# Performance work log

Hardware: AMD Instinct MI355X
Metric: run time of the kernel (lower is better)

The kernel has to match this reference:

```python
import jax, jax.numpy as jnp
import numpy as np

N_NODES = 100000

def _sage_conv(x, src, dst, W_l, b_l, W_r):
    # PyG SAGEConv(aggr='mean'): out = lin_l(mean_{j in N(i)} x_j) + lin_r(x_i)
    agg = jax.ops.segment_sum(x[src], dst, num_segments=N_NODES)          # [N, F]
    cnt = jax.ops.segment_sum(jnp.ones_like(dst, dtype=x.dtype), dst,
                              num_segments=N_NODES)                        # [N]
    mean = agg / jnp.maximum(cnt, 1.0)[:, None]
    return mean @ W_l + b_l + x @ W_r

def setup_inputs() -> dict:
    key = jax.random.key(0)
    ks = jax.random.split(key, 10)
    F_in, H = 128, 16
    E, P = 1600000, 2000000
    x = jax.random.normal(ks[0], (N_NODES, F_in), dtype=jnp.float32)
    edge_index = jax.random.randint(ks[1], (2, E), 0, N_NODES, dtype=jnp.int64)
    decode_index = jax.random.randint(ks[2], (2, P), 0, N_NODES, dtype=jnp.int64)
    s1 = 1.0 / np.sqrt(F_in)
    s2 = 1.0 / np.sqrt(H)
    W1l = jax.random.uniform(ks[3], (F_in, H), jnp.float32, -s1, s1)
    b1 = jax.random.uniform(ks[4], (H,), jnp.float32, -s1, s1)
    W1r = jax.random.uniform(ks[5], (F_in, H), jnp.float32, -s1, s1)
    W2l = jax.random.uniform(ks[6], (H, H), jnp.float32, -s2, s2)
    b2 = jax.random.uniform(ks[7], (H,), jnp.float32, -s2, s2)
    W2r = jax.random.uniform(ks[8], (H, H), jnp.float32, -s2, s2)
    return {"x": x, "W1l": W1l, "b1": b1, "W1r": W1r,
            "W2l": W2l, "b2": b2, "W2r": W2r,
            "edge_index": edge_index, "decode_index": decode_index}

def reference(x, W1l, b1, W1r, W2l, b2, W2r, edge_index, decode_index):
    src, dst = edge_index[0], edge_index[1]
    h = _sage_conv(x, src, dst, W1l, b1, W1r)          # conv1
    h = jax.nn.relu(h)                                  # relu (dropout: eval -> identity)
    h = _sage_conv(h, src, dst, W2l, b2, W2r)           # conv2
    logits = jnp.sum(h[decode_index[0]] * h[decode_index[1]], axis=1)  # [P]
    return jax.nn.sigmoid(logits)
```

## Files before the change

### kernel.cpp

```cpp
#include <hip/hip_runtime.h>
#include <hip/hip_fp16.h>

#define N_NODES 100000
#define F_IN 128
#define H 16
#define NBIN 391
#define BINCAP 4608
#define ECHUNK 4096

__global__ void __launch_bounds__(512) k_init(int* __restrict__ binCur) {
  int t = threadIdx.x;
  if (t < NBIN) binCur[t] = t * BINCAP;
}

__global__ void __launch_bounds__(256) k_lin1(
    const float* __restrict__ x, const float* __restrict__ W1l,
    const float* __restrict__ W1r, __half* __restrict__ y1l,
    float* __restrict__ y1r) {
  __shared__ float red[2 * H * 128];
  int t = threadIdx.x;
  int part = __builtin_amdgcn_readfirstlane(t >> 7);
  int ln = t & 127;
  int n = blockIdx.x * 128 + ln;
  int nc = (n < N_NODES) ? n : (N_NODES - 1);
  const float4* xr = (const float4*)(x + (size_t)nc * F_IN + part * (F_IN / 2));
  float4 xv[16];
#pragma unroll
  for (int j = 0; j < 16; ++j) xv[j] = xr[j];
  const float* Wl = W1l + part * (F_IN / 2) * H;
  const float* Wr = W1r + part * (F_IN / 2) * H;
  float al[H], ar[H];
#pragma unroll
  for (int c = 0; c < H; ++c) { al[c] = 0.f; ar[c] = 0.f; }
#pragma unroll
  for (int j = 0; j < 16; ++j) {
    float xs[4] = {xv[j].x, xv[j].y, xv[j].z, xv[j].w};
#pragma unroll
    for (int jj = 0; jj < 4; ++jj) {
      int k = j * 4 + jj;
#pragma unroll
      for (int c = 0; c < H; ++c) {
        al[c] = fmaf(xs[jj], Wl[k * H + c], al[c]);
        ar[c] = fmaf(xs[jj], Wr[k * H + c], ar[c]);
      }
    }
  }
  if (part == 1) {
#pragma unroll
    for (int c = 0; c < H; ++c) {
      red[c * 128 + ln] = al[c];
      red[(H + c) * 128 + ln] = ar[c];
    }
  }
  __syncthreads();
  if (part == 0 && n < N_NODES) {
#pragma unroll
    for (int c = 0; c < H; ++c) {
      al[c] += red[c * 128 + ln];
      ar[c] += red[(H + c) * 128 + ln];
    }
    __half2 hp[8];
#pragma unroll
    for (int q = 0; q < 8; ++q) hp[q] = __floats2half2_rn(al[2 * q], al[2 * q + 1]);
    uint4* ol = (uint4*)(y1l + (size_t)n * H);
    ol[0] = *(uint4*)&hp[0];
    ol[1] = *(uint4*)&hp[4];
    float4* orr = (float4*)(y1r + (size_t)n * H);
#pragma unroll
    for (int q = 0; q < 4; ++q)
      orr[q] = make_float4(ar[4 * q], ar[4 * q + 1], ar[4 * q + 2], ar[4 * q + 3]);
  }
}

__global__ void __launch_bounds__(512) k_binfill(
    const int* __restrict__ src, const int* __restrict__ dst,
    int* __restrict__ binCur, int* __restrict__ recs, int E) {
  __shared__ int hist[512];
  __shared__ int gbase[512];
  __shared__ int cnt2[512];
  int t = threadIdx.x;
  hist[t] = 0;
  cnt2[t] = 0;
  __syncthreads();
  int base = blockIdx.x * ECHUNK;
  int rec[8], bin[8];
#pragma unroll
  for (int j = 0; j < 8; ++j) {
    int e = base + j * 512 + t;
    if (e < E) {
      int s = src[e];
      int d = dst[e];
      rec[j] = (s << 8) | (d & 255);
      bin[j] = d >> 8;
      atomicAdd(&hist[bin[j]], 1);
    } else {
      bin[j] = -1;
    }
  }
  __syncthreads();
  if (t < NBIN) {
    int c = hist[t];
    gbase[t] = (c > 0) ? atomicAdd(&binCur[t], c) : 0;
  }
  __syncthreads();
#pragma unroll
  for (int j = 0; j < 8; ++j) {
    if (bin[j] >= 0) {
      int loc = atomicAdd(&cnt2[bin[j]], 1);
      int slot = gbase[bin[j]] + loc;
      if (slot < (bin[j] + 1) * BINCAP)
        recs[slot] = rec[j];
    }
  }
}

__global__ void __launch_bounds__(512) k_binsort(
    int* __restrict__ recs, const int* __restrict__ binCur,
    int* __restrict__ deg, int* __restrict__ rowBeg) {
  __shared__ int lrec[BINCAP];
  __shared__ int srtg[BINCAP];
  __shared__ int hist[256];
  __shared__ int off[256];
  __shared__ int cur[256];
  int t = threadIdx.x;
  int b = blockIdx.x;
  int rbase = b * BINCAP;
  int R = binCur[b] - rbase;
  if (R > BINCAP) R = BINCAP;
  if (t < 256) hist[t] = 0;
  __syncthreads();
#pragma unroll
  for (int j = 0; j < 9; ++j) {
    int idx = j * 512 + t;
    if (idx < R) {
      int r = recs[rbase + idx];
      lrec[idx] = r;
      atomicAdd(&hist[r & 255], 1);
    }
  }
  __syncthreads();
  if (t < 256) off[t] = hist[t];
  __syncthreads();
  for (int o = 1; o < 256; o <<= 1) {
    int u = 0;
    if (t < 256 && t >= o) u = off[t - o];
    __syncthreads();
    if (t < 256) off[t] += u;
    __syncthreads();
  }
  if (t < 256) {
    int ex = off[t] - hist[t];
    cur[t] = ex;
    int n = (b << 8) + t;
    if (n < N_NODES) {
      deg[n] = hist[t];
      rowBeg[n] = rbase + ex;
    }
  }
  __syncthreads();
#pragma unroll
  for (int j = 0; j < 9; ++j) {
    int idx = j * 512 + t;
    if (idx < R) {
      int r = lrec[idx];
      int slot = atomicAdd(&cur[r & 255], 1);
      srtg[slot] = r;
    }
  }
  __syncthreads();
#pragma unroll
  for (int j = 0; j < 9; ++j) {
    int idx = j * 512 + t;
    if (idx < R) {
      int r = srtg[idx];
      int node = r & 255;
      int ex = off[node] - hist[node];
      int cnt = hist[node];
      int rank = 0;
      for (int k = ex; k < ex + cnt; ++k) {
        int v = srtg[k];
        rank += (v < r) || (v == r && k < idx);
      }
      lrec[ex + rank] = r >> 8;
    }
  }
  __syncthreads();
#pragma unroll
  for (int j = 0; j < 9; ++j) {
    int idx = j * 512 + t;
    if (idx < R) recs[rbase + idx] = lrec[idx];
  }
}

__global__ void __launch_bounds__(256) k_gather1(
    const int* __restrict__ srcSorted, const int* __restrict__ deg,
    const int* __restrict__ rowBeg, const __half* __restrict__ y1l,
    const float* __restrict__ y1r, const float* __restrict__ b1,
    const float* __restrict__ W2l, const float* __restrict__ W2r,
    __half* __restrict__ z2l, float* __restrict__ z2r) {
  int tid = blockIdx.x * 256 + threadIdx.x;
  int n = tid >> 2;
  int q = tid & 3;
  if (n >= N_NODES) return;
  int beg = rowBeg[n];
  int dg = deg[n];
  int end = beg + dg;
  float acc0 = 0.f, acc1 = 0.f, acc2 = 0.f, acc3 = 0.f;
  int i = beg;
  for (; i + 4 <= end; i += 4) {
    int sq = srcSorted[i + q];
#pragma unroll
    for (int j = 0; j < 4; ++j) {
      int sj = __shfl(sq, j, 4);
      uint2 v = *(const uint2*)(y1l + (size_t)sj * H + q * 4);
      float2 p0 = __half22float2(*(const __half2*)&v.x);
      float2 p1 = __half22float2(*(const __half2*)&v.y);
      acc0 += p0.x; acc1 += p0.y; acc2 += p1.x; acc3 += p1.y;
    }
  }
  for (; i < end; ++i) {
    int sj = srcSorted[i];
    uint2 v = *(const uint2*)(y1l + (size_t)sj * H + q * 4);
    float2 p0 = __half22float2(*(const __half2*)&v.x);
    float2 p1 = __half22float2(*(const __half2*)&v.y);
    acc0 += p0.x; acc1 += p0.y; acc2 += p1.x; acc3 += p1.y;
  }
  float inv = 1.f / fmaxf((float)dg, 1.f);
  float4 yr = *(const float4*)(y1r + (size_t)n * H + q * 4);
  float4 bb = *(const float4*)(b1 + q * 4);
  float h1x = fmaxf(fmaf(acc0, inv, bb.x + yr.x), 0.f);
  float h1y = fmaxf(fmaf(acc1, inv, bb.y + yr.y), 0.f);
  float h1z = fmaxf(fmaf(acc2, inv, bb.z + yr.z), 0.f);
  float h1w = fmaxf(fmaf(acc3, inv, bb.w + yr.w), 0.f);
  float zl0 = 0.f, zl1 = 0.f, zl2 = 0.f, zl3 = 0.f;
  float zr0 = 0.f, zr1 = 0.f, zr2 = 0.f, zr3 = 0.f;
#pragma unroll
  for (int sl = 0; sl < 4; ++sl) {
    float hx = __shfl(h1x, sl, 4);
    float hy = __shfl(h1y, sl, 4);
    float hz = __shfl(h1z, sl, 4);
    float hw = __shfl(h1w, sl, 4);
    float hk4[4] = {hx, hy, hz, hw};
#pragma unroll
    for (int j = 0; j < 4; ++j) {
      int k = sl * 4 + j;
      float4 wl = *(const float4*)(W2l + k * H + q * 4);
      float4 wr = *(const float4*)(W2r + k * H + q * 4);
      float hk = hk4[j];
      zl0 = fmaf(hk, wl.x, zl0); zl1 = fmaf(hk, wl.y, zl1);
      zl2 = fmaf(hk, wl.z, zl2); zl3 = fmaf(hk, wl.w, zl3);
      zr0 = fmaf(hk, wr.x, zr0); zr1 = fmaf(hk, wr.y, zr1);
      zr2 = fmaf(hk, wr.z, zr2); zr3 = fmaf(hk, wr.w, zr3);
    }
  }
  __half2 hl0 = __floats2half2_rn(zl0, zl1);
  __half2 hl1 = __floats2half2_rn(zl2, zl3);
  uint2 pk;
  pk.x = *(unsigned int*)&hl0;
  pk.y = *(unsigned int*)&hl1;
  *(uint2*)(z2l + (size_t)n * H + q * 4) = pk;
  *(float4*)(z2r + (size_t)n * H + q * 4) = make_float4(zr0, zr1, zr2, zr3);
}

__global__ void __launch_bounds__(256) k_gather2(
    const int* __restrict__ srcSorted, const int* __restrict__ deg,
    const int* __restrict__ rowBeg, const __half* __restrict__ z2l,
    const float* __restrict__ z2r, const float* __restrict__ b2,
    __half* __restrict__ h2) {
  int tid = blockIdx.x * 256 + threadIdx.x;
  int n = tid >> 2;
  int q = tid & 3;
  if (n >= N_NODES) return;
  int beg = rowBeg[n];
  int dg = deg[n];
  int end = beg + dg;
  float acc0 = 0.f, acc1 = 0.f, acc2 = 0.f, acc3 = 0.f;
  int i = beg;
  for (; i + 4 <= end; i += 4) {
    int sq = srcSorted[i + q];
#pragma unroll
    for (int j = 0; j < 4; ++j) {
      int sj = __shfl(sq, j, 4);
      uint2 v = *(const uint2*)(z2l + (size_t)sj * H + q * 4);
      float2 p0 = __half22float2(*(const __half2*)&v.x);
      float2 p1 = __half22float2(*(const __half2*)&v.y);
      acc0 += p0.x; acc1 += p0.y; acc2 += p1.x; acc3 += p1.y;
    }
  }
  for (; i < end; ++i) {
    int sj = srcSorted[i];
    uint2 v = *(const uint2*)(z2l + (size_t)sj * H + q * 4);
    float2 p0 = __half22float2(*(const __half2*)&v.x);
    float2 p1 = __half22float2(*(const __half2*)&v.y);
    acc0 += p0.x; acc1 += p0.y; acc2 += p1.x; acc3 += p1.y;
  }
  float inv = 1.f / fmaxf((float)dg, 1.f);
  float4 zr = *(const float4*)(z2r + (size_t)n * H + q * 4);
  float4 bb = *(const float4*)(b2 + q * 4);
  float v0 = fmaf(acc0, inv, bb.x + zr.x);
  float v1 = fmaf(acc1, inv, bb.y + zr.y);
  float v2 = fmaf(acc2, inv, bb.z + zr.z);
  float v3 = fmaf(acc3, inv, bb.w + zr.w);
  __half2 h0 = __floats2half2_rn(v0, v1);
  __half2 h1 = __floats2half2_rn(v2, v3);
  uint2 pk;
  pk.x = *(unsigned int*)&h0;
  pk.y = *(unsigned int*)&h1;
  *(uint2*)(h2 + (size_t)n * H + q * 4) = pk;
}

__device__ inline float dot8h(uint4 u, uint4 v) {
  float acc = 0.f;
  const unsigned int* uw = (const unsigned int*)&u;
  const unsigned int* vw = (const unsigned int*)&v;
#pragma unroll
  for (int j = 0; j < 4; ++j) {
    float2 a = __half22float2(*(const __half2*)&uw[j]);
    float2 b = __half22float2(*(const __half2*)&vw[j]);
    acc = fmaf(a.x, b.x, acc);
    acc = fmaf(a.y, b.y, acc);
  }
  return acc;
}

__global__ void __launch_bounds__(256) k_decode(
    const int* __restrict__ ps, const int* __restrict__ pd,
    const __half* __restrict__ h2, float* __restrict__ out, int P) {
  int p = blockIdx.x * 256 + threadIdx.x;
  if (p >= P) return;
  int a = ps[p];
  int b = pd[p];
  const uint4* ha = (const uint4*)(h2 + (size_t)a * H);
  const uint4* hb = (const uint4*)(h2 + (size_t)b * H);
  uint4 u0 = ha[0], u1 = ha[1];
  uint4 v0 = hb[0], v1 = hb[1];
  float acc = dot8h(u0, v0) + dot8h(u1, v1);
  out[p] = 1.f / (1.f + __expf(-acc));
}

extern "C" void kernel_launch(void* const* d_in, const int* in_sizes, int n_in,
                              void* d_out, int out_size, void* d_ws, size_t ws_size,
                              hipStream_t stream) {
  const float* x   = (const float*)d_in[0];
  const float* W1l = (const float*)d_in[1];
  const float* b1  = (const float*)d_in[2];
  const float* W1r = (const float*)d_in[3];
  const float* W2l = (const float*)d_in[4];
  const float* b2  = (const float*)d_in[5];
  const float* W2r = (const float*)d_in[6];
  const int* ei = (const int*)d_in[7];
  const int* di = (const int*)d_in[8];
  const int E = in_sizes[7] / 2;
  const int P = in_sizes[8] / 2;

  const size_t NF = (size_t)N_NODES * H;
  __half* y1l = (__half*)d_ws;
  __half* h2  = y1l;
  __half* z2l = y1l + NF;
  float*  y1r = (float*)(z2l + NF);
  float*  z2r = y1r;
  int* recs   = (int*)(y1r + NF);
  int* binCur = recs + (size_t)NBIN * BINCAP;
  int* deg    = binCur + 512;
  int* rowBeg = deg + N_NODES;

  const int lin1Blocks = (N_NODES + 127) / 128;
  const int fillBlocks = (E + ECHUNK - 1) / ECHUNK;
  const int gatherBlocks = ((N_NODES * 4) + 255) / 256;

  k_init<<<1, 512, 0, stream>>>(binCur);
  k_lin1<<<lin1Blocks, 256, 0, stream>>>(x, W1l, W1r, y1l, y1r);
  k_binfill<<<fillBlocks, 512, 0, stream>>>(ei, ei + E, binCur, recs, E);
  k_binsort<<<NBIN, 512, 0, stream>>>(recs, binCur, deg, rowBeg);
  k_gather1<<<gatherBlocks, 256, 0, stream>>>(recs, deg, rowBeg, y1l, y1r,
                                              b1, W2l, W2r, z2l, z2r);
  k_gather2<<<gatherBlocks, 256, 0, stream>>>(recs, deg, rowBeg, z2l, z2r,
                                              b2, h2);
  k_decode<<<(P + 255) / 256, 256, 0, stream>>>(di, di + P, h2, (float*)d_out, P);
}
```

Measured before the change: 226.2 us.

## Use int16 fixed-point features and drop per-node edge sorting

Intermediate neighbour features are stored as int16 fixed point (scale 4096) instead of fp16, and the gathers accumulate them with exact integer adds. Because integer sums give the same result in any order, the O(deg^2) per-node rank sort in the bin kernel is removed. Edges are now only grouped by destination and written straight to global memory. This drops the extra shared buffer and the quadratic ranking loop, at the cost of a fixed quantisation range that can clip or lose precision for large or small activations.

```diff
diff --git a/kernel.cpp b/kernel.cpp
--- a/kernel.cpp
+++ b/kernel.cpp
@@ -7,6 +7,14 @@
 #define NBIN 391
 #define BINCAP 4608
 #define ECHUNK 4096
+#define QSCALE 4096.0f
+#define QINV (1.0f / 4096.0f)
+
+__device__ inline unsigned int packi16(float a, float b) {
+  int ia = __float2int_rn(fminf(fmaxf(a * QSCALE, -32767.f), 32767.f));
+  int ib = __float2int_rn(fminf(fmaxf(b * QSCALE, -32767.f), 32767.f));
+  return (unsigned int)((ia & 0xffff) | (ib << 16));
+}
 
 __global__ void __launch_bounds__(512) k_init(int* __restrict__ binCur) {
   int t = threadIdx.x;
@@ -15,7 +23,7 @@
 
 __global__ void __launch_bounds__(256) k_lin1(
     const float* __restrict__ x, const float* __restrict__ W1l,
-    const float* __restrict__ W1r, __half* __restrict__ y1l,
+    const float* __restrict__ W1r, unsigned short* __restrict__ y1l,
     float* __restrict__ y1r) {
   __shared__ float red[2 * H * 128];
   int t = threadIdx.x;
@@ -59,12 +67,14 @@
       al[c] += red[c * 128 + ln];
       ar[c] += red[(H + c) * 128 + ln];
     }
-    __half2 hp[8];
-#pragma unroll
-    for (int q = 0; q < 8; ++q) hp[q] = __floats2half2_rn(al[2 * q], al[2 * q + 1]);
+    uint4 w0, w1;
+    w0.x = packi16(al[0], al[1]);  w0.y = packi16(al[2], al[3]);
+    w0.z = packi16(al[4], al[5]);  w0.w = packi16(al[6], al[7]);
+    w1.x = packi16(al[8], al[9]);  w1.y = packi16(al[10], al[11]);
+    w1.z = packi16(al[12], al[13]); w1.w = packi16(al[14], al[15]);
     uint4* ol = (uint4*)(y1l + (size_t)n * H);
-    ol[0] = *(uint4*)&hp[0];
-    ol[1] = *(uint4*)&hp[4];
+    ol[0] = w0;
+    ol[1] = w1;
     float4* orr = (float4*)(y1r + (size_t)n * H);
 #pragma unroll
     for (int q = 0; q < 4; ++q)
@@ -114,11 +124,10 @@
   }
 }
 
-__global__ void __launch_bounds__(512) k_binsort(
+__global__ void __launch_bounds__(512) k_group(
     int* __restrict__ recs, const int* __restrict__ binCur,
     int* __restrict__ deg, int* __restrict__ rowBeg) {
   __shared__ int lrec[BINCAP];
-  __shared__ int srtg[BINCAP];
   __shared__ int hist[256];
   __shared__ int off[256];
   __shared__ int cur[256];
@@ -164,40 +173,17 @@
     if (idx < R) {
       int r = lrec[idx];
       int slot = atomicAdd(&cur[r & 255], 1);
-      srtg[slot] = r;
-    }
-  }
-  __syncthreads();
-#pragma unroll
-  for (int j = 0; j < 9; ++j) {
-    int idx = j * 512 + t;
-    if (idx < R) {
-      int r = srtg[idx];
-      int node = r & 255;
-      int ex = off[node] - hist[node];
-      int cnt = hist[node];
-      int rank = 0;
-      for (int k = ex; k < ex + cnt; ++k) {
-        int v = srtg[k];
-        rank += (v < r) || (v == r && k < idx);
-      }
-      lrec[ex + rank] = r >> 8;
-    }
-  }
-  __syncthreads();
-#pragma unroll
-  for (int j = 0; j < 9; ++j) {
-    int idx = j * 512 + t;
-    if (idx < R) recs[rbase + idx] = lrec[idx];
+      recs[rbase + slot] = r >> 8;
+    }
   }
 }
 
 __global__ void __launch_bounds__(256) k_gather1(
     const int* __restrict__ srcSorted, const int* __restrict__ deg,
-    const int* __restrict__ rowBeg, const __half* __restrict__ y1l,
+    const int* __restrict__ rowBeg, const unsigned short* __restrict__ y1l,
     const float* __restrict__ y1r, const float* __restrict__ b1,
     const float* __restrict__ W2l, const float* __restrict__ W2r,
-    __half* __restrict__ z2l, float* __restrict__ z2r) {
+    unsigned short* __restrict__ z2l, float* __restrict__ z2r) {
   int tid = blockIdx.x * 256 + threadIdx.x;
   int n = tid >> 2;
   int q = tid & 3;
@@ -205,7 +191,7 @@
   int beg = rowBeg[n];
   int dg = deg[n];
   int end = beg + dg;
-  float acc0 = 0.f, acc1 = 0.f, acc2 = 0.f, acc3 = 0.f;
+  int acc0 = 0, acc1 = 0, acc2 = 0, acc3 = 0;
   int i = beg;
   for (; i + 4 <= end; i += 4) {
     int sq = srcSorted[i + q];
@@ -213,25 +199,27 @@
     for (int j = 0; j < 4; ++j) {
       int sj = __shfl(sq, j, 4);
       uint2 v = *(const uint2*)(y1l + (size_t)sj * H + q * 4);
-      float2 p0 = __half22float2(*(const __half2*)&v.x);
-      float2 p1 = __half22float2(*(const __half2*)&v.y);
-      acc0 += p0.x; acc1 += p0.y; acc2 += p1.x; acc3 += p1.y;
+      acc0 += ((int)(v.x << 16)) >> 16;
+      acc1 += ((int)v.x) >> 16;
+      acc2 += ((int)(v.y << 16)) >> 16;
+      acc3 += ((int)v.y) >> 16;
     }
   }
   for (; i < end; ++i) {
     int sj = srcSorted[i];
     uint2 v = *(const uint2*)(y1l + (size_t)sj * H + q * 4);
-    float2 p0 = __half22float2(*(const __half2*)&v.x);
-    float2 p1 = __half22float2(*(const __half2*)&v.y);
-    acc0 += p0.x; acc1 += p0.y; acc2 += p1.x; acc3 += p1.y;
-  }
-  float inv = 1.f / fmaxf((float)dg, 1.f);
+    acc0 += ((int)(v.x << 16)) >> 16;
+    acc1 += ((int)v.x) >> 16;
+    acc2 += ((int)(v.y << 16)) >> 16;
+    acc3 += ((int)v.y) >> 16;
+  }
+  float s = (1.f / fmaxf((float)dg, 1.f)) * QINV;
   float4 yr = *(const float4*)(y1r + (size_t)n * H + q * 4);
   float4 bb = *(const float4*)(b1 + q * 4);
-  float h1x = fmaxf(fmaf(acc0, inv, bb.x + yr.x), 0.f);
-  float h1y = fmaxf(fmaf(acc1, inv, bb.y + yr.y), 0.f);
-  float h1z = fmaxf(fmaf(acc2, inv, bb.z + yr.z), 0.f);
-  float h1w = fmaxf(fmaf(acc3, inv, bb.w + yr.w), 0.f);
+  float h1x = fmaxf(fmaf((float)acc0, s, bb.x + yr.x), 0.f);
+  float h1y = fmaxf(fmaf((float)acc1, s, bb.y + yr.y), 0.f);
+  float h1z = fmaxf(fmaf((float)acc2, s, bb.z + yr.z), 0.f);
+  float h1w = fmaxf(fmaf((float)acc3, s, bb.w + yr.w), 0.f);
   float zl0 = 0.f, zl1 = 0.f, zl2 = 0.f, zl3 = 0.f;
   float zr0 = 0.f, zr1 = 0.f, zr2 = 0.f, zr3 = 0.f;
 #pragma unroll
@@ -253,18 +241,16 @@
       zr2 = fmaf(hk, wr.z, zr2); zr3 = fmaf(hk, wr.w, zr3);
     }
   }
-  __half2 hl0 = __floats2half2_rn(zl0, zl1);
-  __half2 hl1 = __floats2half2_rn(zl2, zl3);
   uint2 pk;
-  pk.x = *(unsigned int*)&hl0;
-  pk.y = *(unsigned int*)&hl1;
+  pk.x = packi16(zl0, zl1);
+  pk.y = packi16(zl2, zl3);
   *(uint2*)(z2l + (size_t)n * H + q * 4) = pk;
   *(float4*)(z2r + (size_t)n * H + q * 4) = make_float4(zr0, zr1, zr2, zr3);
 }
 
 __global__ void __launch_bounds__(256) k_gather2(
     const int* __restrict__ srcSorted, const int* __restrict__ deg,
-    const int* __restrict__ rowBeg, const __half* __restrict__ z2l,
+    const int* __restrict__ rowBeg, const unsigned short* __restrict__ z2l,
     const float* __restrict__ z2r, const float* __restrict__ b2,
     __half* __restrict__ h2) {
   int tid = blockIdx.x * 256 + threadIdx.x;
@@ -274,7 +260,7 @@
   int beg = rowBeg[n];
   int dg = deg[n];
   int end = beg + dg;
-  float acc0 = 0.f, acc1 = 0.f, acc2 = 0.f, acc3 = 0.f;
+  int acc0 = 0, acc1 = 0, acc2 = 0, acc3 = 0;
   int i = beg;
   for (; i + 4 <= end; i += 4) {
     int sq = srcSorted[i + q];
@@ -282,25 +268,27 @@
     for (int j = 0; j < 4; ++j) {
       int sj = __shfl(sq, j, 4);
       uint2 v = *(const uint2*)(z2l + (size_t)sj * H + q * 4);
-      float2 p0 = __half22float2(*(const __half2*)&v.x);
-      float2 p1 = __half22float2(*(const __half2*)&v.y);
-      acc0 += p0.x; acc1 += p0.y; acc2 += p1.x; acc3 += p1.y;
+      acc0 += ((int)(v.x << 16)) >> 16;
+      acc1 += ((int)v.x) >> 16;
+      acc2 += ((int)(v.y << 16)) >> 16;
+      acc3 += ((int)v.y) >> 16;
     }
   }
   for (; i < end; ++i) {
     int sj = srcSorted[i];
     uint2 v = *(const uint2*)(z2l + (size_t)sj * H + q * 4);
-    float2 p0 = __half22float2(*(const __half2*)&v.x);
-    float2 p1 = __half22float2(*(const __half2*)&v.y);
-    acc0 += p0.x; acc1 += p0.y; acc2 += p1.x; acc3 += p1.y;
-  }
-  float inv = 1.f / fmaxf((float)dg, 1.f);
+    acc0 += ((int)(v.x << 16)) >> 16;
+    acc1 += ((int)v.x) >> 16;
+    acc2 += ((int)(v.y << 16)) >> 16;
+    acc3 += ((int)v.y) >> 16;
+  }
+  float s = (1.f / fmaxf((float)dg, 1.f)) * QINV;
   float4 zr = *(const float4*)(z2r + (size_t)n * H + q * 4);
   float4 bb = *(const float4*)(b2 + q * 4);
-  float v0 = fmaf(acc0, inv, bb.x + zr.x);
-  float v1 = fmaf(acc1, inv, bb.y + zr.y);
-  float v2 = fmaf(acc2, inv, bb.z + zr.z);
-  float v3 = fmaf(acc3, inv, bb.w + zr.w);
+  float v0 = fmaf((float)acc0, s, bb.x + zr.x);
+  float v1 = fmaf((float)acc1, s, bb.y + zr.y);
+  float v2 = fmaf((float)acc2, s, bb.z + zr.z);
+  float v3 = fmaf((float)acc3, s, bb.w + zr.w);
   __half2 h0 = __floats2half2_rn(v0, v1);
   __half2 h1 = __floats2half2_rn(v2, v3);
   uint2 pk;
@@ -354,9 +342,9 @@
   const int P = in_sizes[8] / 2;
 
   const size_t NF = (size_t)N_NODES * H;
-  __half* y1l = (__half*)d_ws;
-  __half* h2  = y1l;
-  __half* z2l = y1l + NF;
+  unsigned short* y1l = (unsigned short*)d_ws;
+  __half*         h2  = (__half*)y1l;
+  unsigned short* z2l = y1l + NF;
   float*  y1r = (float*)(z2l + NF);
   float*  z2r = y1r;
   int* recs   = (int*)(y1r + NF);
@@ -371,7 +359,7 @@
   k_init<<<1, 512, 0, stream>>>(binCur);
   k_lin1<<<lin1Blocks, 256, 0, stream>>>(x, W1l, W1r, y1l, y1r);
   k_binfill<<<fillBlocks, 512, 0, stream>>>(ei, ei + E, binCur, recs, E);
-  k_binsort<<<NBIN, 512, 0, stream>>>(recs, binCur, deg, rowBeg);
+  k_group<<<NBIN, 512, 0, stream>>>(recs, binCur, deg, rowBeg);
   k_gather1<<<gatherBlocks, 256, 0, stream>>>(recs, deg, rowBeg, y1l, y1r,
                                               b1, W2l, W2r, z2l, z2r);
   k_gather2<<<gatherBlocks, 256, 0, stream>>>(recs, deg, rowBeg, z2l, z2r,
```

Result: no change. 225.4 us (-0.3%).
